# Optimization experiments

Hardware: AMD Instinct MI355X
Metric: run time of the kernel (lower is better)

## Reference

```python
import jax, jax.numpy as jnp
import numpy as np

SCALE = 30.0
MARGIN = 0.5
COS_M = float(np.cos(MARGIN))
SIN_M = float(np.sin(MARGIN))
TH = float(np.cos(np.pi - MARGIN))
MM = float(np.sin(np.pi - MARGIN) * MARGIN)
LN_EPS = 1e-7

B, S, H = 16, 2048, 1024
N_SPANS = 64
N_CLASSES = 4096


def setup_inputs() -> dict:
    key = jax.random.key(0)
    k1, k2, k3, k4, k5 = jax.random.split(key, 5)
    encoder_layer = jax.random.normal(k1, (B, S, H), dtype=jnp.float32)
    ln_gamma = jnp.ones((H,), jnp.float32)
    ln_beta = jnp.zeros((H,), jnp.float32)
    # xavier-uniform-like init for arcface head weight [out, in]
    limit = float(np.sqrt(6.0 / (N_CLASSES + H)))
    arc_weight = jax.random.uniform(k2, (N_CLASSES, H), jnp.float32, -limit, limit)
    heads = jax.random.randint(k3, (B, N_SPANS), 0, S - 32).astype(jnp.int32)
    lens = jax.random.randint(k4, (B, N_SPANS), 1, 33).astype(jnp.int32)
    tails = heads + lens  # guaranteed head < tail <= S
    labels = jax.random.randint(k5, (B, N_SPANS), 0, N_CLASSES).astype(jnp.int32)
    return {
        "encoder_layer": encoder_layer,
        "ln_gamma": ln_gamma,
        "ln_beta": ln_beta,
        "arc_weight": arc_weight,
        "span_head_idxs": heads,
        "span_tail_idxs": tails,
        "labels": labels,
    }


def _span_mean(encoder_layer, heads, tails):
    # fused ragged segment-mean via inclusive prefix sums over the seq dim
    # csum: [B, S+1, H], csum[b, t] = sum of encoder_layer[b, :t]
    csum = jnp.concatenate(
        [jnp.zeros_like(encoder_layer[:, :1]), jnp.cumsum(encoder_layer, axis=1)], axis=1
    )
    gather = lambda idx: jnp.take_along_axis(csum, idx[:, :, None].astype(jnp.int32), axis=1)
    sums = gather(tails) - gather(heads)  # [B, n_spans, H]
    counts = (tails - heads).astype(encoder_layer.dtype)[:, :, None]
    return sums / counts


def _layer_norm(x, gamma, beta):
    mu = jnp.mean(x, axis=-1, keepdims=True)
    var = jnp.mean(jnp.square(x - mu), axis=-1, keepdims=True)
    return (x - mu) * jax.lax.rsqrt(var + LN_EPS) * gamma + beta


def _l2norm(x):
    return x / jnp.maximum(jnp.linalg.norm(x, axis=-1, keepdims=True), 1e-12)


def reference(encoder_layer, ln_gamma, ln_beta, arc_weight, span_head_idxs, span_tail_idxs, labels):
    emb = _span_mean(encoder_layer, span_head_idxs, span_tail_idxs)  # [B, n_spans, H]
    emb = _layer_norm(emb, ln_gamma, ln_beta)
    emb = emb.reshape(-1, emb.shape[-1])  # [B*n_spans, H]
    lab = labels.reshape(-1)
    # ArcMarginProduct: cosine similarity
    cosine = (_l2norm(emb) @ _l2norm(arc_weight).T).astype(jnp.float32)  # [N, C]
    sine = jnp.sqrt(jnp.clip(1.0 - jnp.square(cosine), 0.0))
    phi = cosine * COS_M - sine * SIN_M
    phi = jnp.where(cosine > TH, phi, cosine - MM)
    onehot = jax.nn.one_hot(lab, cosine.shape[-1], dtype=cosine.dtype)
    logits = (onehot * phi + (1.0 - onehot) * cosine) * SCALE
    # mean cross entropy (all labels valid, ignore_index unused)
    logp = jax.nn.log_softmax(logits, axis=-1)
    nll = -jnp.take_along_axis(logp, lab[:, None].astype(jnp.int32), axis=1)[:, 0]
    return jnp.mean(nll)
```

## Files before the change

kernel.cpp:

```cpp
#include <hip/hip_runtime.h>
#include <math.h>

#define B_     16
#define S_     2048
#define H_     1024
#define NS_    64
#define NC_    4096
#define NROWS  1024
#define NTILES 32

#define SCALE_ 30.0f
#define COS_M_ 0.8775825618903728f
#define SIN_M_ 0.479425538604203f
#define TH_    (-0.8775825618903728f)
#define MM_    0.2397127693021015f
#define LN_EPS_ 1e-7f


__device__ __forceinline__ unsigned short f2bf(float f) {
    union { float f; unsigned int u; } v; v.f = f;
    unsigned int r = v.u + 0x7fffu + ((v.u >> 16) & 1u);
    return (unsigned short)(r >> 16);
}

__device__ __forceinline__ float block_sum(float v) {
    __shared__ float sb[4];
    #pragma unroll
    for (int off = 32; off > 0; off >>= 1) v += __shfl_down(v, off, 64);
    if ((threadIdx.x & 63) == 0) sb[threadIdx.x >> 6] = v;
    __syncthreads();
    float r = sb[0] + sb[1] + sb[2] + sb[3];
    __syncthreads();
    return r;
}

__device__ __forceinline__ void gload16(const void* g, void* l) {
    __builtin_amdgcn_global_load_lds(
        (const __attribute__((address_space(1))) unsigned int*)g,
        (__attribute__((address_space(3))) unsigned int*)l,
        16, 0, 0);
}

typedef short bf16x8 __attribute__((ext_vector_type(8)));
typedef float f32x4  __attribute__((ext_vector_type(4)));

__global__ __launch_bounds__(256) void fused_norm_kernel(
    const float* __restrict__ enc,
    const float* __restrict__ gamma,
    const float* __restrict__ beta,
    const int*   __restrict__ heads,
    const int*   __restrict__ tails,
    const float* __restrict__ W,
    unsigned short* __restrict__ embn,
    unsigned short* __restrict__ Wn,
    unsigned int*   __restrict__ cnt)
{
    const int tid = threadIdx.x;
    if (blockIdx.x == 0 && tid == 0) *cnt = 0u;

    if (blockIdx.x < NROWS) {
        const int span = blockIdx.x;
        const int b    = span >> 6;
        const int head = heads[span];
        const int tail = tails[span];
        const int cnt_ = tail - head;

        const float4* base = (const float4*)(enc + ((size_t)b * S_ + head) * H_) + tid;
        float4 a0 = {0.f,0.f,0.f,0.f}, a1 = a0, a2 = a0, a3 = a0;
        int s = 0;
        for (; s + 4 <= cnt_; s += 4) {
            float4 x0 = base[(size_t)(s + 0) * (H_ / 4)];
            float4 x1 = base[(size_t)(s + 1) * (H_ / 4)];
            float4 x2 = base[(size_t)(s + 2) * (H_ / 4)];
            float4 x3 = base[(size_t)(s + 3) * (H_ / 4)];
            a0.x += x0.x; a0.y += x0.y; a0.z += x0.z; a0.w += x0.w;
            a1.x += x1.x; a1.y += x1.y; a1.z += x1.z; a1.w += x1.w;
            a2.x += x2.x; a2.y += x2.y; a2.z += x2.z; a2.w += x2.w;
            a3.x += x3.x; a3.y += x3.y; a3.z += x3.z; a3.w += x3.w;
        }
        for (; s < cnt_; ++s) {
            float4 x = base[(size_t)s * (H_ / 4)];
            a0.x += x.x; a0.y += x.y; a0.z += x.z; a0.w += x.w;
        }
        const float inv = 1.0f / (float)cnt_;
        float v0 = (a0.x + a1.x + a2.x + a3.x) * inv;
        float v1 = (a0.y + a1.y + a2.y + a3.y) * inv;
        float v2 = (a0.z + a1.z + a2.z + a3.z) * inv;
        float v3 = (a0.w + a1.w + a2.w + a3.w) * inv;

        float mu = block_sum(v0 + v1 + v2 + v3) * (1.0f / H_);
        float d0 = v0 - mu, d1 = v1 - mu, d2 = v2 - mu, d3 = v3 - mu;
        float var = block_sum(d0*d0 + d1*d1 + d2*d2 + d3*d3) * (1.0f / H_);
        float rstd = rsqrtf(var + LN_EPS_);

        const float4 g4 = ((const float4*)gamma)[tid];
        const float4 b4 = ((const float4*)beta)[tid];
        float y0 = d0 * rstd * g4.x + b4.x;
        float y1 = d1 * rstd * g4.y + b4.y;
        float y2 = d2 * rstd * g4.z + b4.z;
        float y3 = d3 * rstd * g4.w + b4.w;

        float ss = block_sum(y0*y0 + y1*y1 + y2*y2 + y3*y3);
        float invn = 1.0f / fmaxf(sqrtf(ss), 1e-12f);

        ushort4 o;
        o.x = f2bf(y0 * invn); o.y = f2bf(y1 * invn);
        o.z = f2bf(y2 * invn); o.w = f2bf(y3 * invn);
        *(ushort4*)(embn + (size_t)span * H_ + tid * 4) = o;
    } else {
        const int row = blockIdx.x - NROWS;
        float4 x = ((const float4*)(W + (size_t)row * H_))[tid];
        float ss = block_sum(x.x*x.x + x.y*x.y + x.z*x.z + x.w*x.w);
        float invn = 1.0f / fmaxf(sqrtf(ss), 1e-12f);
        ushort4 o;
        o.x = f2bf(x.x * invn); o.y = f2bf(x.y * invn);
        o.z = f2bf(x.z * invn); o.w = f2bf(x.w * invn);
        *(ushort4*)(Wn + (size_t)row * H_ + tid * 4) = o;
    }
}

__global__ __launch_bounds__(256, 1) void gemm_ce_kernel(
    const unsigned short* __restrict__ A,
    const unsigned short* __restrict__ Bw,
    const int*   __restrict__ labels,
    float* __restrict__ tmax,
    float* __restrict__ tsum,
    float* __restrict__ glab)
{
    __shared__ short As[3][128 * 64];
    __shared__ short Bs[3][128 * 64];
    __shared__ float smx[2][128];
    __shared__ float ssm[2][128];

    const int bid = blockIdx.y * 8 + blockIdx.x;
    const int swz = (bid & 7) * 32 + (bid >> 3);
    const int m0  = (swz & 7) * 128;
    const int nt  = swz >> 3;
    const int n0  = nt * 128;

    const int tid  = threadIdx.x;
    const int lane = tid & 63;
    const int w    = tid >> 6;
    const int wm   = (w & 1) * 64;
    const int wnh  = w >> 1;
    const int wn   = wnh * 64;
    const int lrow = lane & 15;
    const int q    = lane >> 4;
    const int xr   = lrow & 7;

    f32x4 acc[4][4];
    #pragma unroll
    for (int i = 0; i < 4; ++i)
        #pragma unroll
        for (int j = 0; j < 4; ++j)
            acc[i][j] = (f32x4){0.f, 0.f, 0.f, 0.f};

    auto stage = [&](int bsel, int k0) {
        #pragma unroll
        for (int h = 0; h < 4; ++h) {
            const int s   = tid + h * 256;
            const int row = s >> 3;
            const int s16 = (s & 7) ^ (row & 7);
            gload16(A  + (size_t)(m0 + row) * 1024 + k0 + s16 * 8, &As[bsel][s * 8]);
            gload16(Bw + (size_t)(n0 + row) * 1024 + k0 + s16 * 8, &Bs[bsel][s * 8]);
        }
    };

    auto compute = [&](int bsel) {
        #pragma unroll
        for (int kk = 0; kk < 2; ++kk) {
            const int c16 = ((kk << 2) | q) ^ xr;
            bf16x8 af[4], bfr[4];
            #pragma unroll
            for (int i = 0; i < 4; ++i)
                af[i] = *(const bf16x8*)(&As[bsel][(wm + i * 16 + lrow) * 64 + c16 * 8]);
            #pragma unroll
            for (int j = 0; j < 4; ++j)
                bfr[j] = *(const bf16x8*)(&Bs[bsel][(wn + j * 16 + lrow) * 64 + c16 * 8]);
            #pragma unroll
            for (int i = 0; i < 4; ++i)
                #pragma unroll
                for (int j = 0; j < 4; ++j)
                    acc[i][j] = __builtin_amdgcn_mfma_f32_16x16x32_bf16(af[i], bfr[j], acc[i][j], 0, 0, 0);
        }
    };

    stage(0, 0);
    stage(1, 64);
    asm volatile("s_waitcnt vmcnt(8)" ::: "memory");
    __builtin_amdgcn_s_barrier();
    __builtin_amdgcn_sched_barrier(0);

    int cur = 0, nxt = 1, fut = 2;
    for (int t = 0; t < 14; ++t) {
        stage(fut, (t + 2) * 64);
        compute(cur);
        asm volatile("s_waitcnt vmcnt(8)" ::: "memory");
        __builtin_amdgcn_s_barrier();
        __builtin_amdgcn_sched_barrier(0);
        const int tmp = cur; cur = nxt; nxt = fut; fut = tmp;
    }
    compute(cur);
    asm volatile("s_waitcnt vmcnt(0)" ::: "memory");
    __builtin_amdgcn_s_barrier();
    __builtin_amdgcn_sched_barrier(0);
    compute(nxt);


    int lab[4][4];
    #pragma unroll
    for (int i = 0; i < 4; ++i)
        #pragma unroll
        for (int r2 = 0; r2 < 4; ++r2)
            lab[i][r2] = labels[m0 + wm + i * 16 + q * 4 + r2];

    #pragma unroll
    for (int i = 0; i < 4; ++i)
        #pragma unroll
        for (int r2 = 0; r2 < 4; ++r2) {
            const int gcol_base = n0 + wn;
            #pragma unroll
            for (int j = 0; j < 4; ++j) {
                const int col = gcol_base + j * 16 + lrow;
                float c = acc[i][j][r2];
                float logit;
                if (col == lab[i][r2]) {
                    float sine = sqrtf(fmaxf(1.0f - c * c, 0.0f));
                    float phi  = c * COS_M_ - sine * SIN_M_;
                    logit = ((c > TH_) ? phi : (c - MM_)) * SCALE_;
                    glab[m0 + wm + i * 16 + q * 4 + r2] = logit;
                } else {
                    logit = c * SCALE_;
                }
                acc[i][j][r2] = logit;
            }
        }

    float mrow[4][4];
    #pragma unroll
    for (int i = 0; i < 4; ++i)
        #pragma unroll
        for (int r2 = 0; r2 < 4; ++r2) {
            float m = fmaxf(fmaxf(acc[i][0][r2], acc[i][1][r2]),
                            fmaxf(acc[i][2][r2], acc[i][3][r2]));
            #pragma unroll
            for (int mk = 1; mk <= 8; mk <<= 1)
                m = fmaxf(m, __shfl_xor(m, mk, 64));
            mrow[i][r2] = m;
        }

    if (lrow == 0) {
        #pragma unroll
        for (int i = 0; i < 4; ++i)
            #pragma unroll
            for (int r2 = 0; r2 < 4; ++r2)
                smx[wnh][wm + i * 16 + q * 4 + r2] = mrow[i][r2];
    }
    __syncthreads();
    float M[4][4];
    #pragma unroll
    for (int i = 0; i < 4; ++i)
        #pragma unroll
        for (int r2 = 0; r2 < 4; ++r2)
            M[i][r2] = fmaxf(mrow[i][r2], smx[wnh ^ 1][wm + i * 16 + q * 4 + r2]);

    float srow[4][4];
    #pragma unroll
    for (int i = 0; i < 4; ++i)
        #pragma unroll
        for (int r2 = 0; r2 < 4; ++r2) {
            float s = expf(acc[i][0][r2] - M[i][r2]) + expf(acc[i][1][r2] - M[i][r2])
                    + expf(acc[i][2][r2] - M[i][r2]) + expf(acc[i][3][r2] - M[i][r2]);
            #pragma unroll
            for (int mk = 1; mk <= 8; mk <<= 1)
                s += __shfl_xor(s, mk, 64);
            srow[i][r2] = s;
        }
    if (lrow == 0) {
        #pragma unroll
        for (int i = 0; i < 4; ++i)
            #pragma unroll
            for (int r2 = 0; r2 < 4; ++r2)
                ssm[wnh][wm + i * 16 + q * 4 + r2] = srow[i][r2];
    }
    __syncthreads();
    if (wnh == 0 && lrow == 0) {
        #pragma unroll
        for (int i = 0; i < 4; ++i)
            #pragma unroll
            for (int r2 = 0; r2 < 4; ++r2) {
                const int rl = wm + i * 16 + q * 4 + r2;
                const int R  = m0 + rl;
                tmax[(size_t)R * NTILES + nt] = M[i][r2];
                tsum[(size_t)R * NTILES + nt] = srow[i][r2] + ssm[1][rl];
            }
    }
}

__global__ __launch_bounds__(256) void combine_kernel(
    const float* __restrict__ tmax,
    const float* __restrict__ tsum,
    const float* __restrict__ glab,
    float* __restrict__ nll,
    float* __restrict__ out,
    unsigned int* __restrict__ cnt)
{
    __shared__ int s_last;
    const int tid = threadIdx.x;
    const int row = blockIdx.x * 256 + tid;

    const float4* mx4 = (const float4*)(tmax + (size_t)row * NTILES);
    const float4* sm4 = (const float4*)(tsum + (size_t)row * NTILES);
    float4 mv[8], sv[8];
    #pragma unroll
    for (int k = 0; k < 8; ++k) { mv[k] = mx4[k]; sv[k] = sm4[k]; }

    float gm = -1e30f;
    #pragma unroll
    for (int k = 0; k < 8; ++k)
        gm = fmaxf(gm, fmaxf(fmaxf(mv[k].x, mv[k].y), fmaxf(mv[k].z, mv[k].w)));

    float se = 0.f;
    #pragma unroll
    for (int k = 0; k < 8; ++k) {
        se += sv[k].x * expf(mv[k].x - gm);
        se += sv[k].y * expf(mv[k].y - gm);
        se += sv[k].z * expf(mv[k].z - gm);
        se += sv[k].w * expf(mv[k].w - gm);
    }
    nll[row] = logf(se) + gm - glab[row];

    if (tid == 0) {
        __threadfence();
        s_last = (atomicAdd(cnt, 1u) == (NROWS / 256) - 1);
    }
    __syncthreads();
    if (s_last) {
        __threadfence();
        float s = 0.f;
        #pragma unroll
        for (int t = 0; t < 4; ++t) s += nll[tid + t * 256];
        float tot = block_sum(s);
        if (tid == 0) out[0] = tot * (1.0f / NROWS);
    }
}

extern "C" void kernel_launch(void* const* d_in, const int* in_sizes, int n_in,
                              void* d_out, int out_size, void* d_ws, size_t ws_size,
                              hipStream_t stream) {
    const float* enc    = (const float*)d_in[0];
    const float* gamma  = (const float*)d_in[1];
    const float* beta   = (const float*)d_in[2];
    const float* W      = (const float*)d_in[3];
    const int*   heads  = (const int*)d_in[4];
    const int*   tails  = (const int*)d_in[5];
    const int*   labels = (const int*)d_in[6];
    float* out = (float*)d_out;

    char* ws = (char*)d_ws;
    unsigned short* embn = (unsigned short*)(ws);
    unsigned short* Wn   = (unsigned short*)(ws + (2u  << 20));
    float* tmax          = (float*)        (ws + (10u << 20));
    float* tsum          = (float*)        (ws + (10u << 20) + (128u<<10));
    float* glab          = (float*)        (ws + (10u << 20) + (256u<<10));
    float* nllbuf        = (float*)        (ws + (10u << 20) + (260u<<10));
    unsigned int* cnt    = (unsigned int*) (ws + (10u << 20) + (264u<<10));

    fused_norm_kernel<<<NROWS + NC_, 256, 0, stream>>>(enc, gamma, beta, heads, tails, W, embn, Wn, cnt);
    dim3 g3(8, 32);
    gemm_ce_kernel <<<g3, 256, 0, stream>>>(embn, Wn, labels, tmax, tsum, glab);
    combine_kernel <<<NROWS / 256, 256, 0, stream>>>(tmax, tsum, glab, nllbuf, out, cnt);
}
```

Baseline: 228.7 us.

## Fuse norm, GEMM-CE, and combine into one cooperative persistent kernel

Merges the three kernels into a single cooperative launch of 256 blocks. The blocks first loop over the span-mean/LayerNorm and weight-normalization tasks, then do a grid-wide sync, run the GEMM with the fused ArcFace CE partials, and the last block to finish does the final combine and mean. This removes two kernel launches and the inter-kernel gaps. In exchange, the norm phase now runs on only 256 resident blocks with launch bounds of one block per SM, which may lower memory parallelism, and it adds grid-sync overhead.

```diff
diff --git a/kernel.cpp b/kernel.cpp
--- a/kernel.cpp
+++ b/kernel.cpp
@@ -1,5 +1,8 @@
 #include <hip/hip_runtime.h>
+#include <hip/hip_cooperative_groups.h>
 #include <math.h>
+
+namespace cg = cooperative_groups;
 
 #define B_     16
 #define S_     2048
@@ -8,6 +11,7 @@
 #define NC_    4096
 #define NROWS  1024
 #define NTILES 32
+#define GRID_  256
 
 #define SCALE_ 30.0f
 #define COS_M_ 0.8775825618903728f
@@ -44,303 +48,297 @@
 typedef short bf16x8 __attribute__((ext_vector_type(8)));
 typedef float f32x4  __attribute__((ext_vector_type(4)));
 
-__global__ __launch_bounds__(256) void fused_norm_kernel(
+__global__ __launch_bounds__(256, 1) void mega_kernel(
     const float* __restrict__ enc,
     const float* __restrict__ gamma,
     const float* __restrict__ beta,
     const int*   __restrict__ heads,
     const int*   __restrict__ tails,
     const float* __restrict__ W,
+    const int*   __restrict__ labels,
     unsigned short* __restrict__ embn,
     unsigned short* __restrict__ Wn,
-    unsigned int*   __restrict__ cnt)
-{
-    const int tid = threadIdx.x;
-    if (blockIdx.x == 0 && tid == 0) *cnt = 0u;
-
-    if (blockIdx.x < NROWS) {
-        const int span = blockIdx.x;
-        const int b    = span >> 6;
-        const int head = heads[span];
-        const int tail = tails[span];
-        const int cnt_ = tail - head;
-
-        const float4* base = (const float4*)(enc + ((size_t)b * S_ + head) * H_) + tid;
-        float4 a0 = {0.f,0.f,0.f,0.f}, a1 = a0, a2 = a0, a3 = a0;
-        int s = 0;
-        for (; s + 4 <= cnt_; s += 4) {
-            float4 x0 = base[(size_t)(s + 0) * (H_ / 4)];
-            float4 x1 = base[(size_t)(s + 1) * (H_ / 4)];
-            float4 x2 = base[(size_t)(s + 2) * (H_ / 4)];
-            float4 x3 = base[(size_t)(s + 3) * (H_ / 4)];
-            a0.x += x0.x; a0.y += x0.y; a0.z += x0.z; a0.w += x0.w;
-            a1.x += x1.x; a1.y += x1.y; a1.z += x1.z; a1.w += x1.w;
-            a2.x += x2.x; a2.y += x2.y; a2.z += x2.z; a2.w += x2.w;
-            a3.x += x3.x; a3.y += x3.y; a3.z += x3.z; a3.w += x3.w;
-        }
-        for (; s < cnt_; ++s) {
-            float4 x = base[(size_t)s * (H_ / 4)];
-            a0.x += x.x; a0.y += x.y; a0.z += x.z; a0.w += x.w;
-        }
-        const float inv = 1.0f / (float)cnt_;
-        float v0 = (a0.x + a1.x + a2.x + a3.x) * inv;
-        float v1 = (a0.y + a1.y + a2.y + a3.y) * inv;
-        float v2 = (a0.z + a1.z + a2.z + a3.z) * inv;
-        float v3 = (a0.w + a1.w + a2.w + a3.w) * inv;
-
-        float mu = block_sum(v0 + v1 + v2 + v3) * (1.0f / H_);
-        float d0 = v0 - mu, d1 = v1 - mu, d2 = v2 - mu, d3 = v3 - mu;
-        float var = block_sum(d0*d0 + d1*d1 + d2*d2 + d3*d3) * (1.0f / H_);
-        float rstd = rsqrtf(var + LN_EPS_);
-
-        const float4 g4 = ((const float4*)gamma)[tid];
-        const float4 b4 = ((const float4*)beta)[tid];
-        float y0 = d0 * rstd * g4.x + b4.x;
-        float y1 = d1 * rstd * g4.y + b4.y;
-        float y2 = d2 * rstd * g4.z + b4.z;
-        float y3 = d3 * rstd * g4.w + b4.w;
-
-        float ss = block_sum(y0*y0 + y1*y1 + y2*y2 + y3*y3);
-        float invn = 1.0f / fmaxf(sqrtf(ss), 1e-12f);
-
-        ushort4 o;
-        o.x = f2bf(y0 * invn); o.y = f2bf(y1 * invn);
-        o.z = f2bf(y2 * invn); o.w = f2bf(y3 * invn);
-        *(ushort4*)(embn + (size_t)span * H_ + tid * 4) = o;
-    } else {
-        const int row = blockIdx.x - NROWS;
-        float4 x = ((const float4*)(W + (size_t)row * H_))[tid];
-        float ss = block_sum(x.x*x.x + x.y*x.y + x.z*x.z + x.w*x.w);
-        float invn = 1.0f / fmaxf(sqrtf(ss), 1e-12f);
-        ushort4 o;
-        o.x = f2bf(x.x * invn); o.y = f2bf(x.y * invn);
-        o.z = f2bf(x.z * invn); o.w = f2bf(x.w * invn);
-        *(ushort4*)(Wn + (size_t)row * H_ + tid * 4) = o;
-    }
-}
-
-__global__ __launch_bounds__(256, 1) void gemm_ce_kernel(
-    const unsigned short* __restrict__ A,
-    const unsigned short* __restrict__ Bw,
-    const int*   __restrict__ labels,
     float* __restrict__ tmax,
     float* __restrict__ tsum,
-    float* __restrict__ glab)
+    float* __restrict__ glab,
+    float* __restrict__ out,
+    unsigned int* __restrict__ cnt)
 {
     __shared__ short As[3][128 * 64];
     __shared__ short Bs[3][128 * 64];
     __shared__ float smx[2][128];
     __shared__ float ssm[2][128];
-
-    const int bid = blockIdx.y * 8 + blockIdx.x;
-    const int swz = (bid & 7) * 32 + (bid >> 3);
-    const int m0  = (swz & 7) * 128;
-    const int nt  = swz >> 3;
-    const int n0  = nt * 128;
-
-    const int tid  = threadIdx.x;
-    const int lane = tid & 63;
-    const int w    = tid >> 6;
-    const int wm   = (w & 1) * 64;
-    const int wnh  = w >> 1;
-    const int wn   = wnh * 64;
-    const int lrow = lane & 15;
-    const int q    = lane >> 4;
-    const int xr   = lrow & 7;
-
-    f32x4 acc[4][4];
-    #pragma unroll
-    for (int i = 0; i < 4; ++i)
-        #pragma unroll
-        for (int j = 0; j < 4; ++j)
-            acc[i][j] = (f32x4){0.f, 0.f, 0.f, 0.f};
-
-    auto stage = [&](int bsel, int k0) {
-        #pragma unroll
-        for (int h = 0; h < 4; ++h) {
-            const int s   = tid + h * 256;
-            const int row = s >> 3;
-            const int s16 = (s & 7) ^ (row & 7);
-            gload16(A  + (size_t)(m0 + row) * 1024 + k0 + s16 * 8, &As[bsel][s * 8]);
-            gload16(Bw + (size_t)(n0 + row) * 1024 + k0 + s16 * 8, &Bs[bsel][s * 8]);
-        }
-    };
-
-    auto compute = [&](int bsel) {
-        #pragma unroll
-        for (int kk = 0; kk < 2; ++kk) {
-            const int c16 = ((kk << 2) | q) ^ xr;
-            bf16x8 af[4], bfr[4];
-            #pragma unroll
-            for (int i = 0; i < 4; ++i)
-                af[i] = *(const bf16x8*)(&As[bsel][(wm + i * 16 + lrow) * 64 + c16 * 8]);
+    __shared__ int   s_last;
+
+    const int bid = blockIdx.x;
+    const int tid = threadIdx.x;
+
+    if (bid == 0 && tid == 0) *cnt = 0u;
+
+    for (int task = bid; task < NROWS + NC_; task += GRID_) {
+        if (task < NROWS) {
+            const int span = task;
+            const int b    = span >> 6;
+            const int head = heads[span];
+            const int tail = tails[span];
+            const int cnt_ = tail - head;
+
+            const float4* base = (const float4*)(enc + ((size_t)b * S_ + head) * H_) + tid;
+            float4 a0 = {0.f,0.f,0.f,0.f}, a1 = a0, a2 = a0, a3 = a0;
+            int s = 0;
+            for (; s + 4 <= cnt_; s += 4) {
+                float4 x0 = base[(size_t)(s + 0) * (H_ / 4)];
+                float4 x1 = base[(size_t)(s + 1) * (H_ / 4)];
+                float4 x2 = base[(size_t)(s + 2) * (H_ / 4)];
+                float4 x3 = base[(size_t)(s + 3) * (H_ / 4)];
+                a0.x += x0.x; a0.y += x0.y; a0.z += x0.z; a0.w += x0.w;
+                a1.x += x1.x; a1.y += x1.y; a1.z += x1.z; a1.w += x1.w;
+                a2.x += x2.x; a2.y += x2.y; a2.z += x2.z; a2.w += x2.w;
+                a3.x += x3.x; a3.y += x3.y; a3.z += x3.z; a3.w += x3.w;
+            }
+            for (; s < cnt_; ++s) {
+                float4 x = base[(size_t)s * (H_ / 4)];
+                a0.x += x.x; a0.y += x.y; a0.z += x.z; a0.w += x.w;
+            }
+            const float inv = 1.0f / (float)cnt_;
+            float v0 = (a0.x + a1.x + a2.x + a3.x) * inv;
+            float v1 = (a0.y + a1.y + a2.y + a3.y) * inv;
+            float v2 = (a0.z + a1.z + a2.z + a3.z) * inv;
+            float v3 = (a0.w + a1.w + a2.w + a3.w) * inv;
+
+            float mu = block_sum(v0 + v1 + v2 + v3) * (1.0f / H_);
+            float d0 = v0 - mu, d1 = v1 - mu, d2 = v2 - mu, d3 = v3 - mu;
+            float var = block_sum(d0*d0 + d1*d1 + d2*d2 + d3*d3) * (1.0f / H_);
+            float rstd = rsqrtf(var + LN_EPS_);
+
+            const float4 g4 = ((const float4*)gamma)[tid];
+            const float4 b4 = ((const float4*)beta)[tid];
+            float y0 = d0 * rstd * g4.x + b4.x;
+            float y1 = d1 * rstd * g4.y + b4.y;
+            float y2 = d2 * rstd * g4.z + b4.z;
+            float y3 = d3 * rstd * g4.w + b4.w;
+
+            float ss = block_sum(y0*y0 + y1*y1 + y2*y2 + y3*y3);
+            float invn = 1.0f / fmaxf(sqrtf(ss), 1e-12f);
+
+            ushort4 o;
+            o.x = f2bf(y0 * invn); o.y = f2bf(y1 * invn);
+            o.z = f2bf(y2 * invn); o.w = f2bf(y3 * invn);
+            *(ushort4*)(embn + (size_t)span * H_ + tid * 4) = o;
+        } else {
+            const int row = task - NROWS;
+            float4 x = ((const float4*)(W + (size_t)row * H_))[tid];
+            float ss = block_sum(x.x*x.x + x.y*x.y + x.z*x.z + x.w*x.w);
+            float invn = 1.0f / fmaxf(sqrtf(ss), 1e-12f);
+            ushort4 o;
+            o.x = f2bf(x.x * invn); o.y = f2bf(x.y * invn);
+            o.z = f2bf(x.z * invn); o.w = f2bf(x.w * invn);
+            *(ushort4*)(Wn + (size_t)row * H_ + tid * 4) = o;
+        }
+    }
+
+    __threadfence();
+    cg::this_grid().sync();
+
+    {
+        const int swz = (bid & 7) * 32 + (bid >> 3);
+        const int m0  = (swz & 7) * 128;
+        const int nt  = swz >> 3;
+        const int n0  = nt * 128;
+
+        const int lane = tid & 63;
+        const int w    = tid >> 6;
+        const int wm   = (w & 1) * 64;
+        const int wnh  = w >> 1;
+        const int wn   = wnh * 64;
+        const int lrow = lane & 15;
+        const int q    = lane >> 4;
+        const int xr   = lrow & 7;
+
+        f32x4 acc[4][4];
+        #pragma unroll
+        for (int i = 0; i < 4; ++i)
             #pragma unroll
             for (int j = 0; j < 4; ++j)
-                bfr[j] = *(const bf16x8*)(&Bs[bsel][(wn + j * 16 + lrow) * 64 + c16 * 8]);
-            #pragma unroll
-            for (int i = 0; i < 4; ++i)
+                acc[i][j] = (f32x4){0.f, 0.f, 0.f, 0.f};
+
+        const unsigned short* A  = embn;
+        const unsigned short* Bw = Wn;
+
+        auto stage = [&](int bsel, int k0) {
+            #pragma unroll
+            for (int h = 0; h < 4; ++h) {
+                const int s   = tid + h * 256;
+                const int row = s >> 3;
+                const int s16 = (s & 7) ^ (row & 7);
+                gload16(A  + (size_t)(m0 + row) * 1024 + k0 + s16 * 8, &As[bsel][s * 8]);
+                gload16(Bw + (size_t)(n0 + row) * 1024 + k0 + s16 * 8, &Bs[bsel][s * 8]);
+            }
+        };
+
+        auto compute = [&](int bsel) {
+            #pragma unroll
+            for (int kk = 0; kk < 2; ++kk) {
+                const int c16 = ((kk << 2) | q) ^ xr;
+                bf16x8 af[4], bfr[4];
+                #pragma unroll
+                for (int i = 0; i < 4; ++i)
+                    af[i] = *(const bf16x8*)(&As[bsel][(wm + i * 16 + lrow) * 64 + c16 * 8]);
                 #pragma unroll
                 for (int j = 0; j < 4; ++j)
-                    acc[i][j] = __builtin_amdgcn_mfma_f32_16x16x32_bf16(af[i], bfr[j], acc[i][j], 0, 0, 0);
-        }
-    };
-
-    stage(0, 0);
-    stage(1, 64);
-    asm volatile("s_waitcnt vmcnt(8)" ::: "memory");
-    __builtin_amdgcn_s_barrier();
-    __builtin_amdgcn_sched_barrier(0);
-
-    int cur = 0, nxt = 1, fut = 2;
-    for (int t = 0; t < 14; ++t) {
-        stage(fut, (t + 2) * 64);
-        compute(cur);
+                    bfr[j] = *(const bf16x8*)(&Bs[bsel][(wn + j * 16 + lrow) * 64 + c16 * 8]);
+                #pragma unroll
+                for (int i = 0; i < 4; ++i)
+                    #pragma unroll
+                    for (int j = 0; j < 4; ++j)
+                        acc[i][j] = __builtin_amdgcn_mfma_f32_16x16x32_bf16(af[i], bfr[j], acc[i][j], 0, 0, 0);
+            }
+        };
+
+        stage(0, 0);
+        stage(1, 64);
         asm volatile("s_waitcnt vmcnt(8)" ::: "memory");
         __builtin_amdgcn_s_barrier();
         __builtin_amdgcn_sched_barrier(0);
-        const int tmp = cur; cur = nxt; nxt = fut; fut = tmp;
+
+        int cur = 0, nxt = 1, fut = 2;
+        for (int t = 0; t < 14; ++t) {
+            stage(fut, (t + 2) * 64);
+            compute(cur);
+            asm volatile("s_waitcnt vmcnt(8)" ::: "memory");
+            __builtin_amdgcn_s_barrier();
+            __builtin_amdgcn_sched_barrier(0);
+            const int tmp = cur; cur = nxt; nxt = fut; fut = tmp;
+        }
+        compute(cur);
+        asm volatile("s_waitcnt vmcnt(0)" ::: "memory");
+        __builtin_amdgcn_s_barrier();
+        __builtin_amdgcn_sched_barrier(0);
+        compute(nxt);
+
+        int lab[4][4];
+        #pragma unroll
+        for (int i = 0; i < 4; ++i)
+            #pragma unroll
+            for (int r2 = 0; r2 < 4; ++r2)
+                lab[i][r2] = labels[m0 + wm + i * 16 + q * 4 + r2];
+
+        #pragma unroll
+        for (int i = 0; i < 4; ++i)
+            #pragma unroll
+            for (int r2 = 0; r2 < 4; ++r2) {
+                const int gcol_base = n0 + wn;
+                #pragma unroll
+                for (int j = 0; j < 4; ++j) {
+                    const int col = gcol_base + j * 16 + lrow;
+                    float c = acc[i][j][r2];
+                    float logit;
+                    if (col == lab[i][r2]) {
+                        float sine = sqrtf(fmaxf(1.0f - c * c, 0.0f));
+                        float phi  = c * COS_M_ - sine * SIN_M_;
+                        logit = ((c > TH_) ? phi : (c - MM_)) * SCALE_;
+                        glab[m0 + wm + i * 16 + q * 4 + r2] = logit;
+                    } else {
+                        logit = c * SCALE_;
+                    }
+                    acc[i][j][r2] = logit;
+                }
+            }
+
+        float mrow[4][4];
+        #pragma unroll
+        for (int i = 0; i < 4; ++i)
+            #pragma unroll
+            for (int r2 = 0; r2 < 4; ++r2) {
+                float m = fmaxf(fmaxf(acc[i][0][r2], acc[i][1][r2]),
+                                fmaxf(acc[i][2][r2], acc[i][3][r2]));
+                #pragma unroll
+                for (int mk = 1; mk <= 8; mk <<= 1)
+                    m = fmaxf(m, __shfl_xor(m, mk, 64));
+                mrow[i][r2] = m;
+            }
+
+        if (lrow == 0) {
+            #pragma unroll
+            for (int i = 0; i < 4; ++i)
+                #pragma unroll
+                for (int r2 = 0; r2 < 4; ++r2)
+                    smx[wnh][wm + i * 16 + q * 4 + r2] = mrow[i][r2];
+        }
+        __syncthreads();
+        float M[4][4];
+        #pragma unroll
+        for (int i = 0; i < 4; ++i)
+            #pragma unroll
+            for (int r2 = 0; r2 < 4; ++r2)
+                M[i][r2] = fmaxf(mrow[i][r2], smx[wnh ^ 1][wm + i * 16 + q * 4 + r2]);
+
+        float srow[4][4];
+        #pragma unroll
+        for (int i = 0; i < 4; ++i)
+            #pragma unroll
+            for (int r2 = 0; r2 < 4; ++r2) {
+                float s = expf(acc[i][0][r2] - M[i][r2]) + expf(acc[i][1][r2] - M[i][r2])
+                        + expf(acc[i][2][r2] - M[i][r2]) + expf(acc[i][3][r2] - M[i][r2]);
+                #pragma unroll
+                for (int mk = 1; mk <= 8; mk <<= 1)
+                    s += __shfl_xor(s, mk, 64);
+                srow[i][r2] = s;
+            }
+        if (lrow == 0) {
+            #pragma unroll
+            for (int i = 0; i < 4; ++i)
+                #pragma unroll
+                for (int r2 = 0; r2 < 4; ++r2)
+                    ssm[wnh][wm + i * 16 + q * 4 + r2] = srow[i][r2];
+        }
+        __syncthreads();
+        if (wnh == 0 && lrow == 0) {
+            #pragma unroll
+            for (int i = 0; i < 4; ++i)
+                #pragma unroll
+                for (int r2 = 0; r2 < 4; ++r2) {
+                    const int rl = wm + i * 16 + q * 4 + r2;
+                    const int R  = m0 + rl;
+                    tmax[(size_t)R * NTILES + nt] = M[i][r2];
+                    tsum[(size_t)R * NTILES + nt] = srow[i][r2] + ssm[1][rl];
+                }
+        }
     }
-    compute(cur);
-    asm volatile("s_waitcnt vmcnt(0)" ::: "memory");
-    __builtin_amdgcn_s_barrier();
-    __builtin_amdgcn_sched_barrier(0);
-    compute(nxt);
-
-
-    int lab[4][4];
-    #pragma unroll
-    for (int i = 0; i < 4; ++i)
-        #pragma unroll
-        for (int r2 = 0; r2 < 4; ++r2)
-            lab[i][r2] = labels[m0 + wm + i * 16 + q * 4 + r2];
-
-    #pragma unroll
-    for (int i = 0; i < 4; ++i)
-        #pragma unroll
-        for (int r2 = 0; r2 < 4; ++r2) {
-            const int gcol_base = n0 + wn;
-            #pragma unroll
-            for (int j = 0; j < 4; ++j) {
-                const int col = gcol_base + j * 16 + lrow;
-                float c = acc[i][j][r2];
-                float logit;
-                if (col == lab[i][r2]) {
-                    float sine = sqrtf(fmaxf(1.0f - c * c, 0.0f));
-                    float phi  = c * COS_M_ - sine * SIN_M_;
-                    logit = ((c > TH_) ? phi : (c - MM_)) * SCALE_;
-                    glab[m0 + wm + i * 16 + q * 4 + r2] = logit;
-                } else {
-                    logit = c * SCALE_;
-                }
-                acc[i][j][r2] = logit;
-            }
-        }
-
-    float mrow[4][4];
-    #pragma unroll
-    for (int i = 0; i < 4; ++i)
-        #pragma unroll
-        for (int r2 = 0; r2 < 4; ++r2) {
-            float m = fmaxf(fmaxf(acc[i][0][r2], acc[i][1][r2]),
-                            fmaxf(acc[i][2][r2], acc[i][3][r2]));
-            #pragma unroll
-            for (int mk = 1; mk <= 8; mk <<= 1)
-                m = fmaxf(m, __shfl_xor(m, mk, 64));
-            mrow[i][r2] = m;
-        }
-
-    if (lrow == 0) {
-        #pragma unroll
-        for (int i = 0; i < 4; ++i)
-            #pragma unroll
-            for (int r2 = 0; r2 < 4; ++r2)
-                smx[wnh][wm + i * 16 + q * 4 + r2] = mrow[i][r2];
-    }
-    __syncthreads();
-    float M[4][4];
-    #pragma unroll
-    for (int i = 0; i < 4; ++i)
-        #pragma unroll
-        for (int r2 = 0; r2 < 4; ++r2)
-            M[i][r2] = fmaxf(mrow[i][r2], smx[wnh ^ 1][wm + i * 16 + q * 4 + r2]);
-
-    float srow[4][4];
-    #pragma unroll
-    for (int i = 0; i < 4; ++i)
-        #pragma unroll
-        for (int r2 = 0; r2 < 4; ++r2) {
-            float s = expf(acc[i][0][r2] - M[i][r2]) + expf(acc[i][1][r2] - M[i][r2])
-                    + expf(acc[i][2][r2] - M[i][r2]) + expf(acc[i][3][r2] - M[i][r2]);
-            #pragma unroll
-            for (int mk = 1; mk <= 8; mk <<= 1)
-                s += __shfl_xor(s, mk, 64);
-            srow[i][r2] = s;
-        }
-    if (lrow == 0) {
-        #pragma unroll
-        for (int i = 0; i < 4; ++i)
-            #pragma unroll
-            for (int r2 = 0; r2 < 4; ++r2)
-                ssm[wnh][wm + i * 16 + q * 4 + r2] = srow[i][r2];
-    }
-    __syncthreads();
-    if (wnh == 0 && lrow == 0) {
-        #pragma unroll
-        for (int i = 0; i < 4; ++i)
-            #pragma unroll
-            for (int r2 = 0; r2 < 4; ++r2) {
-                const int rl = wm + i * 16 + q * 4 + r2;
-                const int R  = m0 + rl;
-                tmax[(size_t)R * NTILES + nt] = M[i][r2];
-                tsum[(size_t)R * NTILES + nt] = srow[i][r2] + ssm[1][rl];
-            }
-    }
-}
-
-__global__ __launch_bounds__(256) void combine_kernel(
-    const float* __restrict__ tmax,
-    const float* __restrict__ tsum,
-    const float* __restrict__ glab,
-    float* __restrict__ nll,
-    float* __restrict__ out,
-    unsigned int* __restrict__ cnt)
-{
-    __shared__ int s_last;
-    const int tid = threadIdx.x;
-    const int row = blockIdx.x * 256 + tid;
-
-    const float4* mx4 = (const float4*)(tmax + (size_t)row * NTILES);
-    const float4* sm4 = (const float4*)(tsum + (size_t)row * NTILES);
-    float4 mv[8], sv[8];
-    #pragma unroll
-    for (int k = 0; k < 8; ++k) { mv[k] = mx4[k]; sv[k] = sm4[k]; }
-
-    float gm = -1e30f;
-    #pragma unroll
-    for (int k = 0; k < 8; ++k)
-        gm = fmaxf(gm, fmaxf(fmaxf(mv[k].x, mv[k].y), fmaxf(mv[k].z, mv[k].w)));
-
-    float se = 0.f;
-    #pragma unroll
-    for (int k = 0; k < 8; ++k) {
-        se += sv[k].x * expf(mv[k].x - gm);
-        se += sv[k].y * expf(mv[k].y - gm);
-        se += sv[k].z * expf(mv[k].z - gm);
-        se += sv[k].w * expf(mv[k].w - gm);
-    }
-    nll[row] = logf(se) + gm - glab[row];
 
     if (tid == 0) {
         __threadfence();
-        s_last = (atomicAdd(cnt, 1u) == (NROWS / 256) - 1);
+        s_last = (atomicAdd(cnt, 1u) == GRID_ - 1);
     }
     __syncthreads();
     if (s_last) {
         __threadfence();
-        float s = 0.f;
-        #pragma unroll
-        for (int t = 0; t < 4; ++t) s += nll[tid + t * 256];
-        float tot = block_sum(s);
+        float acc_nll = 0.f;
+        #pragma unroll
+        for (int t = 0; t < 4; ++t) {
+            const int row = tid + t * 256;
+            const float4* mx4 = (const float4*)(tmax + (size_t)row * NTILES);
+            const float4* sm4 = (const float4*)(tsum + (size_t)row * NTILES);
+            float4 mv[8], sv[8];
+            #pragma unroll
+            for (int k = 0; k < 8; ++k) { mv[k] = mx4[k]; sv[k] = sm4[k]; }
+
+            float gm = -1e30f;
+            #pragma unroll
+            for (int k = 0; k < 8; ++k)
+                gm = fmaxf(gm, fmaxf(fmaxf(mv[k].x, mv[k].y), fmaxf(mv[k].z, mv[k].w)));
+
+            float se = 0.f;
+            #pragma unroll
+            for (int k = 0; k < 8; ++k) {
+                se += sv[k].x * expf(mv[k].x - gm);
+                se += sv[k].y * expf(mv[k].y - gm);
+                se += sv[k].z * expf(mv[k].z - gm);
+                se += sv[k].w * expf(mv[k].w - gm);
+            }
+            acc_nll += logf(se) + gm - glab[row];
+        }
+        float tot = block_sum(acc_nll);
         if (tid == 0) out[0] = tot * (1.0f / NROWS);
     }
 }
@@ -363,11 +361,12 @@
     float* tmax          = (float*)        (ws + (10u << 20));
     float* tsum          = (float*)        (ws + (10u << 20) + (128u<<10));
     float* glab          = (float*)        (ws + (10u << 20) + (256u<<10));
-    float* nllbuf        = (float*)        (ws + (10u << 20) + (260u<<10));
-    unsigned int* cnt    = (unsigned int*) (ws + (10u << 20) + (264u<<10));
-
-    fused_norm_kernel<<<NROWS + NC_, 256, 0, stream>>>(enc, gamma, beta, heads, tails, W, embn, Wn, cnt);
-    dim3 g3(8, 32);
-    gemm_ce_kernel <<<g3, 256, 0, stream>>>(embn, Wn, labels, tmax, tsum, glab);
-    combine_kernel <<<NROWS / 256, 256, 0, stream>>>(tmax, tsum, glab, nllbuf, out, cnt);
-}
+    unsigned int* cnt    = (unsigned int*) (ws + (10u << 20) + (260u<<10));
+
+    void* args[] = { (void*)&enc, (void*)&gamma, (void*)&beta, (void*)&heads,
+                     (void*)&tails, (void*)&W, (void*)&labels, (void*)&embn,
+                     (void*)&Wn, (void*)&tmax, (void*)&tsum, (void*)&glab,
+                     (void*)&out, (void*)&cnt };
+    hipLaunchCooperativeKernel((const void*)mega_kernel, dim3(GRID_), dim3(256),
+                               args, 0, stream);
+}
```

Measured after the change: 349.2 us. +52.6%, slower.
